# Optimization experiments

Measured on AMD Instinct MI355X. Metric: run time of the kernel, lower is better.

Reference implementation:

```python
import jax, jax.numpy as jnp
import numpy as np

DIM = 1024
N_HEADS = 16
HEAD_DIM = DIM // N_HEADS
SCALE = 1.0 / HEAD_DIM ** 0.5


def setup_inputs() -> dict:
    key = jax.random.key(0)
    k1, k2, k3, k4, k5 = jax.random.split(key, 5)
    B, T = 4, 2048
    x = jax.random.normal(k1, (B, T, DIM), dtype=jnp.float32)
    # torch nn.Linear weights: y = x @ W.T + b
    w_qkv = jax.random.normal(k2, (3 * DIM, DIM), dtype=jnp.float32) * 0.02
    b_qkv = jax.random.normal(k3, (3 * DIM,), dtype=jnp.float32) * 0.02
    w_proj = jax.random.normal(k4, (DIM, DIM), dtype=jnp.float32) * 0.02
    b_proj = jax.random.normal(k5, (DIM,), dtype=jnp.float32) * 0.02
    return {"x": x, "w_qkv": w_qkv, "b_qkv": b_qkv, "w_proj": w_proj, "b_proj": b_proj}


def reference(x, w_qkv, b_qkv, w_proj, b_proj):
    B, T, D = x.shape
    qkv = x @ w_qkv.T + b_qkv                              # [B, T, 3D]
    qkv = qkv.reshape(B, T, 3, N_HEADS, HEAD_DIM)
    qkv = jnp.transpose(qkv, (2, 0, 3, 1, 4))              # [3, B, h, T, d]
    q, k, v = qkv[0], qkv[1], qkv[2]
    s = jnp.einsum('bhqd,bhkd->bhqk', q, k) * SCALE        # [B, h, T, T]
    attn = jax.nn.softmax(s, axis=-1)
    out = jnp.einsum('bhqk,bhkd->bqhd', attn, v)           # [B, T, h, d]
    out = out.reshape(B, T, D)
    return out @ w_proj.T + b_proj
```

## Files before the change

### kernel.cpp

```cpp
#include <hip/hip_runtime.h>
#include <stdint.h>

typedef short short8 __attribute__((ext_vector_type(8)));
typedef _Float16 half4 __attribute__((ext_vector_type(4)));
typedef __fp16 fp16x2 __attribute__((ext_vector_type(2)));
typedef unsigned int uint2v __attribute__((ext_vector_type(2)));
typedef float floatx4 __attribute__((ext_vector_type(4)));

#define LOG2E 1.44269504088896340736f
#define QSCALE (0.125f * LOG2E)

static __device__ __forceinline__ unsigned short f2bf(float f) {
  unsigned int u = __float_as_uint(f);
  u += 0x7fffu + ((u >> 16) & 1u);
  return (unsigned short)(u >> 16);
}

static __device__ __forceinline__ float fexp2(float x) {
#if __has_builtin(__builtin_amdgcn_exp2f)
  return __builtin_amdgcn_exp2f(x);
#else
  return exp2f(x);
#endif
}

#define GLD_LDS16(gp, lp)                                                      \
  __builtin_amdgcn_global_load_lds(                                            \
      (const __attribute__((address_space(1))) void*)(gp),                     \
      (__attribute__((address_space(3))) void*)(lp), 16, 0, 0)

__global__ __launch_bounds__(256) void cvt_f32_bf16(
    const float* __restrict__ in, unsigned short* __restrict__ out, int n) {
  int i = (blockIdx.x * 256 + threadIdx.x) * 4;
  if (i >= n) return;
  float4 v = *(const float4*)(in + i);
  ushort4 u;
  u.x = f2bf(v.x); u.y = f2bf(v.y); u.z = f2bf(v.z); u.w = f2bf(v.w);
  *(ushort4*)(out + i) = u;
}

template <int MODE>
__global__ __launch_bounds__(256, 2) void gemm_bt(
    const unsigned short* __restrict__ A, const unsigned short* __restrict__ Bm,
    const float* __restrict__ bias, float* __restrict__ outF,
    unsigned short* __restrict__ qo, unsigned short* __restrict__ ko,
    _Float16* __restrict__ vto, int M, int N, int K) {
  __shared__ unsigned short As[128 * 64];
  __shared__ unsigned short Bs[128 * 64];
  const int tid = threadIdx.x;
  const int w = tid >> 6, l = tid & 63;
  const int lr = l & 15, lg = l >> 4;
  const int nbn = N >> 7;
  const int nwg = gridDim.x;
  const int bid = blockIdx.x;
  const int cpx = nwg >> 3;
  const int swz = (bid & 7) * cpx + (bid >> 3);
  const int bm = swz / nbn, bn = swz % nbn;
  const int wm = w >> 1, wn = w & 1;

  floatx4 acc[4][4];
#pragma unroll
  for (int i = 0; i < 4; ++i)
#pragma unroll
    for (int j = 0; j < 4; ++j) acc[i][j] = (floatx4){0.f, 0.f, 0.f, 0.f};

  for (int k0 = 0; k0 < K; k0 += 64) {
#pragma unroll
    for (int i = 0; i < 4; ++i) {
      int c = i * 256 + tid;
      const unsigned short* ga =
          A + ((size_t)bm * 128 + (c >> 3)) * K + k0 + (c & 7) * 8;
      GLD_LDS16(ga, As + (size_t)(i * 256 + w * 64) * 8);
    }
#pragma unroll
    for (int i = 0; i < 4; ++i) {
      int c = i * 256 + tid;
      const unsigned short* gb =
          Bm + ((size_t)bn * 128 + (c >> 3)) * K + k0 + (c & 7) * 8;
      GLD_LDS16(gb, Bs + (size_t)(i * 256 + w * 64) * 8);
    }
    __syncthreads();
#pragma unroll
    for (int kk = 0; kk < 2; ++kk) {
      short8 af[4], bf[4];
#pragma unroll
      for (int i = 0; i < 4; ++i)
        af[i] = *(const short8*)&As[(wm * 64 + i * 16 + lr) * 64 + kk * 32 + lg * 8];
#pragma unroll
      for (int j = 0; j < 4; ++j)
        bf[j] = *(const short8*)&Bs[(wn * 64 + j * 16 + lr) * 64 + kk * 32 + lg * 8];
#pragma unroll
      for (int i = 0; i < 4; ++i)
#pragma unroll
        for (int j = 0; j < 4; ++j)
          acc[i][j] = __builtin_amdgcn_mfma_f32_16x16x32_bf16(af[i], bf[j],
                                                              acc[i][j], 0, 0, 0);
    }
    __syncthreads();
  }

#pragma unroll
  for (int i = 0; i < 4; ++i) {
    int row0 = bm * 128 + wm * 64 + i * 16 + lg * 4;
#pragma unroll
    for (int j = 0; j < 4; ++j) {
      int col = bn * 128 + wn * 64 + j * 16 + lr;
      float bv = bias[col];
#pragma unroll
      for (int jj = 0; jj < 4; ++jj) {
        float v = acc[i][j][jj] + bv;
        int r = row0 + jj;
        if (MODE == 0) {
          outF[(size_t)r * N + col] = v;
        } else {
          int three = col >> 10, cc = col & 1023;
          int h = cc >> 6, d = cc & 63;
          int b = r >> 11, t = r & 2047;
          if (three == 0)
            qo[(((size_t)(b * 16 + h)) * 2048 + t) * 64 + d] = f2bf(v * QSCALE);
          else if (three == 1)
            ko[(((size_t)(b * 16 + h)) * 2048 + t) * 64 + d] = f2bf(v);
          else
            vto[(((size_t)(b * 16 + h)) * 64 + d) * 2048 + t] = (_Float16)v;
        }
      }
    }
  }
}

__global__ __launch_bounds__(256, 3) void attn_fwd(
    const unsigned short* __restrict__ Qg, const unsigned short* __restrict__ Kg,
    const _Float16* __restrict__ VTg, unsigned short* __restrict__ Og) {
  __shared__ unsigned short Ks[2][64 * 64];
  __shared__ _Float16 Vs[2][64 * 64];

  const int bid0 = blockIdx.x;
  const int bid = (bid0 & 7) * 128 + (bid0 >> 3);
  const int bh = bid >> 4, qt = bid & 15;
  const int b = bh >> 4, hh = bh & 15;
  const int tid = threadIdx.x, w = tid >> 6, l = tid & 63;
  const int l4 = l & 15, g = l >> 4;
  const unsigned short* Q = Qg + (size_t)bh * (2048 * 64);
  const unsigned short* Kp = Kg + (size_t)bh * (2048 * 64);
  const _Float16* VT = VTg + (size_t)bh * (64 * 2048);
  const int qw = qt * 128 + w * 32;

  const int c0 = tid, c1 = 256 + tid;
  const int r0 = c0 >> 3, s0 = (c0 & 7) ^ (r0 & 7);
  const int r1 = c1 >> 3, s1 = (c1 & 7) ^ (r1 & 7);
  const unsigned short* kp0 = Kp + (size_t)r0 * 64 + s0 * 8;
  const unsigned short* kp1 = Kp + (size_t)r1 * 64 + s1 * 8;
  const _Float16* vp0 = VT + (size_t)r0 * 2048 + s0 * 8;
  const _Float16* vp1 = VT + (size_t)r1 * 2048 + s1 * 8;
  unsigned short* ksd0 = &Ks[0][c0 * 8];
  unsigned short* ksd1 = &Ks[0][c1 * 8];
  _Float16* vsd0 = &Vs[0][c0 * 8];
  _Float16* vsd1 = &Vs[0][c1 * 8];

#define STAGE(bufofs, tt)                                                     \
  do {                                                                        \
    GLD_LDS16(kp0 + (size_t)(tt) * 64, ksd0 + (bufofs) * 4096);               \
    GLD_LDS16(kp1 + (size_t)(tt) * 64, ksd1 + (bufofs) * 4096);               \
    GLD_LDS16(vp0 + (tt), vsd0 + (bufofs) * 4096);                            \
    GLD_LDS16(vp1 + (tt), vsd1 + (bufofs) * 4096);                            \
  } while (0)

  const int kb0 = l4 * 64 + ((g ^ (l4 & 7)) * 8);
  const int kb1 = l4 * 64 + (((4 + g) ^ (l4 & 7)) * 8);
  int vb[4];
#pragma unroll
  for (int f = 0; f < 4; ++f)
    vb[f] = l4 * 64 + (((2 * f + (g >> 1)) ^ (l4 & 7)) * 8 + (g & 1) * 4);

  short8 qf[2][2];
#pragma unroll
  for (int qs = 0; qs < 2; ++qs)
#pragma unroll
    for (int c = 0; c < 2; ++c)
      qf[qs][c] =
          *(const short8*)&Q[(size_t)(qw + qs * 16 + l4) * 64 + c * 32 + g * 8];

  floatx4 o[2][4];
#pragma unroll
  for (int qs = 0; qs < 2; ++qs)
#pragma unroll
    for (int db = 0; db < 4; ++db) o[qs][db] = (floatx4){0.f, 0.f, 0.f, 0.f};
  float m[2] = {-__builtin_inff(), -__builtin_inff()};
  float lp[2] = {0.f, 0.f};

  STAGE(0, 0);
  __syncthreads();

#pragma unroll 2
  for (int it = 0; it < 32; ++it) {
    const int cur = it & 1;
    if (it + 1 < 32) STAGE(cur ^ 1, (it + 1) * 64);

    floatx4 s[2][4];
#pragma unroll
    for (int f = 0; f < 4; ++f) {
      short8 kf0 = *(const short8*)&Ks[cur][kb0 + f * 1024];
      short8 kf1 = *(const short8*)&Ks[cur][kb1 + f * 1024];
      floatx4 z = (floatx4){0.f, 0.f, 0.f, 0.f};
      floatx4 t00 = __builtin_amdgcn_mfma_f32_16x16x32_bf16(kf0, qf[0][0], z, 0, 0, 0);
      s[0][f] = __builtin_amdgcn_mfma_f32_16x16x32_bf16(kf1, qf[0][1], t00, 0, 0, 0);
      floatx4 t10 = __builtin_amdgcn_mfma_f32_16x16x32_bf16(kf0, qf[1][0], z, 0, 0, 0);
      s[1][f] = __builtin_amdgcn_mfma_f32_16x16x32_bf16(kf1, qf[1][1], t10, 0, 0, 0);
    }

    half4 pf[2][4];
#pragma unroll
    for (int qs = 0; qs < 2; ++qs) {
      float e[16];
      float rs = 0.f;
#pragma unroll
      for (int f = 0; f < 4; ++f)
#pragma unroll
        for (int jj = 0; jj < 4; ++jj) {
          float pv = fexp2(s[qs][f][jj] - m[qs]);
          e[f * 4 + jj] = pv;
          rs += pv;
        }

      if (!__all(rs <= 256.0f)) {
        float a0 = fmaxf(fmaxf(s[qs][0][0], s[qs][0][1]), fmaxf(s[qs][0][2], s[qs][0][3]));
        float a1 = fmaxf(fmaxf(s[qs][1][0], s[qs][1][1]), fmaxf(s[qs][1][2], s[qs][1][3]));
        float a2 = fmaxf(fmaxf(s[qs][2][0], s[qs][2][1]), fmaxf(s[qs][2][2], s[qs][2][3]));
        float a3 = fmaxf(fmaxf(s[qs][3][0], s[qs][3][1]), fmaxf(s[qs][3][2], s[qs][3][3]));
        float pp = fmaxf(fmaxf(a0, a1), fmaxf(a2, a3));
        pp = fmaxf(pp, __shfl_xor(pp, 16));
        pp = fmaxf(pp, __shfl_xor(pp, 32));
        float mo = m[qs];
        m[qs] = fmaxf(mo, pp);
        float al = fexp2(mo - m[qs]);
        lp[qs] *= al;
#pragma unroll
        for (int jj = 0; jj < 4; ++jj) {
          float alr = __shfl(al, g * 4 + jj);
          o[qs][0][jj] *= alr; o[qs][1][jj] *= alr;
          o[qs][2][jj] *= alr; o[qs][3][jj] *= alr;
        }
        rs = 0.f;
#pragma unroll
        for (int f = 0; f < 4; ++f)
#pragma unroll
          for (int jj = 0; jj < 4; ++jj) {
            float pv = fexp2(s[qs][f][jj] - m[qs]);
            e[f * 4 + jj] = pv;
            rs += pv;
          }
      }
      lp[qs] += rs;

#pragma unroll
      for (int f = 0; f < 4; ++f) {
        fp16x2 plo = __builtin_amdgcn_cvt_pkrtz(e[f * 4 + 0], e[f * 4 + 1]);
        fp16x2 phi = __builtin_amdgcn_cvt_pkrtz(e[f * 4 + 2], e[f * 4 + 3]);
        uint2v u;
        u.x = __builtin_bit_cast(unsigned int, plo);
        u.y = __builtin_bit_cast(unsigned int, phi);
        pf[qs][f] = __builtin_bit_cast(half4, u);
      }
    }

#pragma unroll
    for (int db = 0; db < 4; ++db) {
#pragma unroll
      for (int f = 0; f < 4; ++f) {
        half4 vf = *(const half4*)&Vs[cur][vb[f] + db * 1024];
        o[0][db] = __builtin_amdgcn_mfma_f32_16x16x16f16(pf[0][f], vf, o[0][db], 0, 0, 0);
        o[1][db] = __builtin_amdgcn_mfma_f32_16x16x16f16(pf[1][f], vf, o[1][db], 0, 0, 0);
      }
    }
    __syncthreads();
  }

#pragma unroll
  for (int qs = 0; qs < 2; ++qs) {
    float ls = lp[qs];
    ls += __shfl_xor(ls, 16);
    ls += __shfl_xor(ls, 32);
    float invq = 1.f / ls;
    float inv[4];
#pragma unroll
    for (int jj = 0; jj < 4; ++jj) inv[jj] = __shfl(invq, g * 4 + jj);
#pragma unroll
    for (int db = 0; db < 4; ++db)
#pragma unroll
      for (int jj = 0; jj < 4; ++jj)
        Og[((size_t)b * 2048 + qw + qs * 16 + g * 4 + jj) * 1024 + hh * 64 +
           db * 16 + l4] = f2bf(o[qs][db][jj] * inv[jj]);
  }
#undef STAGE
}

extern "C" void kernel_launch(void* const* d_in, const int* in_sizes, int n_in,
                              void* d_out, int out_size, void* d_ws, size_t ws_size,
                              hipStream_t stream) {
  const float* x = (const float*)d_in[0];
  const float* w_qkv = (const float*)d_in[1];
  const float* b_qkv = (const float*)d_in[2];
  const float* w_proj = (const float*)d_in[3];
  const float* b_proj = (const float*)d_in[4];
  float* out = (float*)d_out;

  char* p = (char*)d_ws;
  unsigned short* xb = (unsigned short*)p;     p += (size_t)8192 * 1024 * 2;
  unsigned short* wqkvb = (unsigned short*)p;  p += (size_t)3072 * 1024 * 2;
  unsigned short* wprojb = (unsigned short*)p; p += (size_t)1024 * 1024 * 2;
  unsigned short* qb = (unsigned short*)p;     p += (size_t)64 * 2048 * 64 * 2;
  unsigned short* kb = (unsigned short*)p;     p += (size_t)64 * 2048 * 64 * 2;
  _Float16* vtb = (_Float16*)p;                p += (size_t)64 * 64 * 2048 * 2;
  unsigned short* attnb = (unsigned short*)p;  p += (size_t)8192 * 1024 * 2;

  cvt_f32_bf16<<<dim3(8192), dim3(256), 0, stream>>>(x, xb, 8192 * 1024);
  cvt_f32_bf16<<<dim3(3072), dim3(256), 0, stream>>>(w_qkv, wqkvb, 3072 * 1024);
  cvt_f32_bf16<<<dim3(1024), dim3(256), 0, stream>>>(w_proj, wprojb, 1024 * 1024);

  gemm_bt<1><<<dim3(64 * 24), dim3(256), 0, stream>>>(
      xb, wqkvb, b_qkv, nullptr, qb, kb, vtb, 8192, 3072, 1024);

  attn_fwd<<<dim3(1024), dim3(256), 0, stream>>>(qb, kb, vtb, attnb);

  gemm_bt<0><<<dim3(64 * 8), dim3(256), 0, stream>>>(
      attnb, wprojb, b_proj, out, nullptr, nullptr, nullptr, 8192, 1024, 1024);
}
```

Measured before the change: 217.8 us.

## Use 16x16x32 f16 MFMA for PV with permuted K row staging

Replaces the sixteen 16x16x16 f16 MFMAs per PV step with eight 16x16x32 f16 MFMAs that take 8-wide fp16 operands. To make the P fragments from the QK^T output line up with the wider K dimension, K rows are loaded into LDS in a permuted order, and V is read as 16-byte half8 vectors. This halves the PV MFMA instruction count and LDS read instructions. It relies on the key-row permutation being consistent between the S layout and the V layout.

```diff
diff --git a/kernel.cpp b/kernel.cpp
--- a/kernel.cpp
+++ b/kernel.cpp
@@ -3,8 +3,10 @@
 
 typedef short short8 __attribute__((ext_vector_type(8)));
 typedef _Float16 half4 __attribute__((ext_vector_type(4)));
+typedef _Float16 half8 __attribute__((ext_vector_type(8)));
 typedef __fp16 fp16x2 __attribute__((ext_vector_type(2)));
 typedef unsigned int uint2v __attribute__((ext_vector_type(2)));
+typedef unsigned int uintx4 __attribute__((ext_vector_type(4)));
 typedef float floatx4 __attribute__((ext_vector_type(4)));
 
 #define LOG2E 1.44269504088896340736f
@@ -145,17 +147,18 @@
   const _Float16* VT = VTg + (size_t)bh * (64 * 2048);
   const int qw = qt * 128 + w * 32;
 
-  const int c0 = tid, c1 = 256 + tid;
-  const int r0 = c0 >> 3, s0 = (c0 & 7) ^ (r0 & 7);
-  const int r1 = c1 >> 3, s1 = (c1 & 7) ^ (r1 & 7);
-  const unsigned short* kp0 = Kp + (size_t)r0 * 64 + s0 * 8;
-  const unsigned short* kp1 = Kp + (size_t)r1 * 64 + s1 * 8;
+  const int r0 = tid >> 3;
+  const int s0 = (tid & 7) ^ (r0 & 7);
+  const int kv0 = (r0 & 16) ? (((r0 & 15) >> 2) * 8 + 4 + (r0 & 3))
+                            : ((r0 >> 2) * 8 + (r0 & 3));
+  const unsigned short* kp0 = Kp + (size_t)kv0 * 64 + s0 * 8;
+  const unsigned short* kp1 = Kp + (size_t)(kv0 + 32) * 64 + s0 * 8;
   const _Float16* vp0 = VT + (size_t)r0 * 2048 + s0 * 8;
-  const _Float16* vp1 = VT + (size_t)r1 * 2048 + s1 * 8;
-  unsigned short* ksd0 = &Ks[0][c0 * 8];
-  unsigned short* ksd1 = &Ks[0][c1 * 8];
-  _Float16* vsd0 = &Vs[0][c0 * 8];
-  _Float16* vsd1 = &Vs[0][c1 * 8];
+  const _Float16* vp1 = VT + (size_t)(r0 + 32) * 2048 + s0 * 8;
+  unsigned short* ksd0 = &Ks[0][tid * 8];
+  unsigned short* ksd1 = &Ks[0][(256 + tid) * 8];
+  _Float16* vsd0 = &Vs[0][tid * 8];
+  _Float16* vsd1 = &Vs[0][(256 + tid) * 8];
 
 #define STAGE(bufofs, tt)                                                     \
   do {                                                                        \
@@ -167,10 +170,10 @@
 
   const int kb0 = l4 * 64 + ((g ^ (l4 & 7)) * 8);
   const int kb1 = l4 * 64 + (((4 + g) ^ (l4 & 7)) * 8);
-  int vb[4];
-#pragma unroll
-  for (int f = 0; f < 4; ++f)
-    vb[f] = l4 * 64 + (((2 * f + (g >> 1)) ^ (l4 & 7)) * 8 + (g & 1) * 4);
+  int vb[2];
+#pragma unroll
+  for (int B = 0; B < 2; ++B)
+    vb[B] = l4 * 64 + (((B * 4 + g) ^ (l4 & 7)) * 8);
 
   short8 qf[2][2];
 #pragma unroll
@@ -208,7 +211,7 @@
       s[1][f] = __builtin_amdgcn_mfma_f32_16x16x32_bf16(kf1, qf[1][1], t10, 0, 0, 0);
     }
 
-    half4 pf[2][4];
+    uint2v pu[2][4];
 #pragma unroll
     for (int qs = 0; qs < 2; ++qs) {
       float e[16];
@@ -256,20 +259,25 @@
       for (int f = 0; f < 4; ++f) {
         fp16x2 plo = __builtin_amdgcn_cvt_pkrtz(e[f * 4 + 0], e[f * 4 + 1]);
         fp16x2 phi = __builtin_amdgcn_cvt_pkrtz(e[f * 4 + 2], e[f * 4 + 3]);
-        uint2v u;
-        u.x = __builtin_bit_cast(unsigned int, plo);
-        u.y = __builtin_bit_cast(unsigned int, phi);
-        pf[qs][f] = __builtin_bit_cast(half4, u);
+        pu[qs][f].x = __builtin_bit_cast(unsigned int, plo);
+        pu[qs][f].y = __builtin_bit_cast(unsigned int, phi);
       }
     }
 
 #pragma unroll
-    for (int db = 0; db < 4; ++db) {
-#pragma unroll
-      for (int f = 0; f < 4; ++f) {
-        half4 vf = *(const half4*)&Vs[cur][vb[f] + db * 1024];
-        o[0][db] = __builtin_amdgcn_mfma_f32_16x16x16f16(pf[0][f], vf, o[0][db], 0, 0, 0);
-        o[1][db] = __builtin_amdgcn_mfma_f32_16x16x16f16(pf[1][f], vf, o[1][db], 0, 0, 0);
+    for (int B = 0; B < 2; ++B) {
+      uintx4 ua0, ua1;
+      ua0.x = pu[0][2 * B].x;     ua0.y = pu[0][2 * B].y;
+      ua0.z = pu[0][2 * B + 1].x; ua0.w = pu[0][2 * B + 1].y;
+      ua1.x = pu[1][2 * B].x;     ua1.y = pu[1][2 * B].y;
+      ua1.z = pu[1][2 * B + 1].x; ua1.w = pu[1][2 * B + 1].y;
+      half8 pa0 = __builtin_bit_cast(half8, ua0);
+      half8 pa1 = __builtin_bit_cast(half8, ua1);
+#pragma unroll
+      for (int db = 0; db < 4; ++db) {
+        half8 vf = *(const half8*)&Vs[cur][vb[B] + db * 1024];
+        o[0][db] = __builtin_amdgcn_mfma_f32_16x16x32_f16(pa0, vf, o[0][db], 0, 0, 0);
+        o[1][db] = __builtin_amdgcn_mfma_f32_16x16x32_f16(pa1, vf, o[1][db], 0, 0, 0);
       }
     }
     __syncthreads();
```

Result: faster. 205.1 us (-5.8%).
